# Performance work log

Hardware: AMD Instinct MI355X
Metric: run time of the kernel (lower is better)

Reference implementation:

```python
import jax, jax.numpy as jnp
import numpy as np

B, L, I, O = 32, 512, 1024, 1024
TMIN, TMAX = -8.0, -2.0


def setup_inputs() -> dict:
    key = jax.random.key(0)
    k1, k2, k3, k4, k5 = jax.random.split(key, 5)
    x = jax.random.normal(k1, (B, L, I), dtype=jnp.float32)
    weight_mean = jax.random.normal(k2, (O, I), dtype=jnp.float32) * 0.02
    # matches torch init: -rand * (tmax - tmin) + tmin
    weight_logvar = -jax.random.uniform(k3, (O, I), dtype=jnp.float32) * (TMAX - TMIN) + TMIN
    bias = jax.random.normal(k4, (O,), dtype=jnp.float32) * 0.02
    # standard-normal reparameterization noise (the torch module's randn)
    noise = jax.random.normal(k5, (B, O, I), dtype=jnp.float32)
    return {"x": x, "weight_mean": weight_mean, "weight_logvar": weight_logvar,
            "bias": bias, "noise": noise}


def reference(x, weight_mean, weight_logvar, bias, noise):
    # per-sample sampled weights: W_b = mean + eps_b * sqrt(exp(logvar))
    w = weight_mean + noise * jnp.exp(0.5 * weight_logvar)  # (B, O, I)
    # bmm(x, W^T) + bias  ->  (B, L, O)
    return jnp.einsum('bli,boi->blo', x, w) + bias
```

## Files before the change

kernel.cpp:

```cpp
#include <hip/hip_runtime.h>
#include <hip/hip_bf16.h>
#include <stdint.h>

#define B_ 32
#define L_ 512
#define I_ 1024
#define O_ 1024
#define NST 32

typedef float  f32x4 __attribute__((ext_vector_type(4)));
typedef float  f32x2 __attribute__((ext_vector_type(2)));
typedef __bf16 bf16x4 __attribute__((ext_vector_type(4)));
typedef __bf16 bf16x8 __attribute__((ext_vector_type(8)));

#define CFENCE() asm volatile("" ::: "memory")
#define BARRIER() do { CFENCE(); __builtin_amdgcn_s_barrier(); CFENCE(); } while (0)
#define LGKM0()  asm volatile("s_waitcnt lgkmcnt(0)" ::: "memory")

__global__ void gen_ms_kernel(const float* __restrict__ wmean, const float* __restrict__ wlv,
                              __bf16* __restrict__ mz, __bf16* __restrict__ sgm)
{
    const int i = blockIdx.x * blockDim.x + threadIdx.x;
    const f32x4 m = *(const f32x4*)(wmean + (size_t)i * 4);
    const f32x4 l = *(const f32x4*)(wlv   + (size_t)i * 4);
    bf16x4 mb, sb;
    #pragma unroll
    for (int e = 0; e < 4; ++e) {
        mb[e] = (__bf16)m[e];
        sb[e] = (__bf16)__expf(0.5f * l[e]);
    }
    *(bf16x4*)(mz  + (size_t)i * 4) = mb;
    *(bf16x4*)(sgm + (size_t)i * 4) = sb;
}

__global__ __launch_bounds__(256, 2) void fused_gemm(const float* __restrict__ x,
                                                     const float* __restrict__ noise,
                                                     const __bf16* __restrict__ mz,
                                                     const __bf16* __restrict__ sgm,
                                                     const float* __restrict__ bias,
                                                     float* __restrict__ out)
{
    __shared__ __align__(16) char smem[33280];

    const int bid = ((int)blockIdx.x & 7) * 128 + ((int)blockIdx.x >> 3);
    const int b   = bid >> 5;
    const int mt  = (bid >> 3) & 3;
    const int nt  = bid & 7;

    const int tid  = threadIdx.x;
    const int wave = tid >> 6, lane = tid & 63;
    const int wr   = wave >> 1;
    const int wc   = wave & 1;
    const int hr   = lane & 15;
    const int kq   = lane >> 4;

    const int r1 = tid >> 2, kc = tid & 3;
    const float*  xg = x     + ((size_t)b * L_ + mt * 128 + r1) * I_ + kc * 8;
    const float*  ng = noise + ((size_t)b * O_ + nt * 128 + r1) * I_ + kc * 8;
    const __bf16* mg = mz    + (size_t)(nt * 128 + r1) * I_ + kc * 8;
    const __bf16* gg = sgm   + (size_t)(nt * 128 + r1) * I_ + kc * 8;
    const size_t H64 = (size_t)64 * I_;
    const int wb = tid * 16;

    f32x4 sa0, sa1, sa2, sa3;
    f32x4 sn0, sn1, sn2, sn3;
    bf16x8 sm0, sm1, sg0, sg1;

#define ISSUE(k0_) do {                                      \
        sa0 = *(const f32x4*)(xg + (k0_));                   \
        sa1 = *(const f32x4*)(xg + (k0_) + 4);               \
        sa2 = *(const f32x4*)(xg + (k0_) + H64);             \
        sa3 = *(const f32x4*)(xg + (k0_) + H64 + 4);         \
        sn0 = *(const f32x4*)(ng + (k0_));                   \
        sn1 = *(const f32x4*)(ng + (k0_) + 4);               \
        sn2 = *(const f32x4*)(ng + (k0_) + H64);             \
        sn3 = *(const f32x4*)(ng + (k0_) + H64 + 4);         \
        sm0 = *(const bf16x8*)(mg + (k0_));                  \
        sm1 = *(const bf16x8*)(mg + (k0_) + H64);            \
        sg0 = *(const bf16x8*)(gg + (k0_));                  \
        sg1 = *(const bf16x8*)(gg + (k0_) + H64);            \
    } while (0)

#define TW(d_) do {                                                         \
        bf16x8 a0_, a1_, w0_, w1_;                                          \
        _Pragma("unroll")                                                   \
        for (int e = 0; e < 4; ++e) {                                       \
            a0_[e]   = (__bf16)sa0[e];  a0_[e+4] = (__bf16)sa1[e];          \
            a1_[e]   = (__bf16)sa2[e];  a1_[e+4] = (__bf16)sa3[e];          \
            w0_[e]   = (__bf16)((float)sm0[e]   + sn0[e] * (float)sg0[e]);  \
            w0_[e+4] = (__bf16)((float)sm0[e+4] + sn1[e] * (float)sg0[e+4]);\
            w1_[e]   = (__bf16)((float)sm1[e]   + sn2[e] * (float)sg1[e]);  \
            w1_[e+4] = (__bf16)((float)sm1[e+4] + sn3[e] * (float)sg1[e+4]);\
        }                                                                   \
        *(bf16x8*)(smem + (d_) * 16384 + wb)               = a0_;           \
        *(bf16x8*)(smem + (d_) * 16384 + wb + 4096)        = a1_;           \
        *(bf16x8*)(smem + (d_) * 16384 + 8192 + wb)        = w0_;           \
        *(bf16x8*)(smem + (d_) * 16384 + 8192 + wb + 4096) = w1_;           \
    } while (0)

    int aoff[4], boff[4];
    #pragma unroll
    for (int f = 0; f < 4; ++f) {
        aoff[f] = (wr * 64 + f * 16 + hr) * 64 + kq * 16;
        boff[f] = 8192 + (wc * 64 + f * 16 + hr) * 64 + kq * 16;
    }

    f32x4 acc[4][4];
    #pragma unroll
    for (int m = 0; m < 4; ++m)
        #pragma unroll
        for (int n = 0; n < 4; ++n)
            acc[m][n] = (f32x4)(0.0f);

    ISSUE(0);
    TW(0);
    ISSUE(32);
    LGKM0();
    BARRIER();

    for (int t = 0; t < NST; ++t) {
        const char* base = smem + (t & 1) * 16384;

        bf16x8 af[4], bfr[4];
        #pragma unroll
        for (int f = 0; f < 4; ++f) {
            af[f]  = *(const bf16x8*)(base + aoff[f]);
            bfr[f] = *(const bf16x8*)(base + boff[f]);
        }

        __builtin_amdgcn_s_setprio(1);
        #pragma unroll
        for (int m = 0; m < 4; ++m)
            #pragma unroll
            for (int n = 0; n < 4; ++n)
                acc[m][n] = __builtin_amdgcn_mfma_f32_16x16x32_bf16(af[m], bfr[n], acc[m][n], 0, 0, 0);
        __builtin_amdgcn_s_setprio(0);

        if (t + 1 < NST) TW((t + 1) & 1);
        if (t + 2 < NST) ISSUE((t + 2) * 32);
        LGKM0();
        BARRIER();
    }
#undef ISSUE
#undef TW

    {
        float* eb = (float*)smem;
        const f32x2 bias2 = *(const f32x2*)(bias + nt * 128 + lane * 2);
        float* ob = out + ((size_t)b * L_ + mt * 128) * O_ + nt * 128;
        #pragma unroll
        for (int r = 0; r < 2; ++r) {
            BARRIER();
            if (wr == r) {
                #pragma unroll
                for (int m = 0; m < 4; ++m)
                    #pragma unroll
                    for (int n = 0; n < 4; ++n) {
                        const int col = wc * 64 + n * 16 + hr;
                        #pragma unroll
                        for (int j = 0; j < 4; ++j)
                            eb[(m * 16 + kq * 4 + j) * 130 + col] = acc[m][n][j];
                    }
            }
            LGKM0();
            BARRIER();
            #pragma unroll
            for (int rr = 0; rr < 16; ++rr) {
                const int row = wave * 16 + rr;
                f32x2 v = *(const f32x2*)&eb[row * 130 + lane * 2];
                v[0] += bias2[0]; v[1] += bias2[1];
                *(f32x2*)&ob[(size_t)(r * 64 + row) * O_ + lane * 2] = v;
            }
        }
    }
}

#define LDSPAD 40
__global__ void bayes_gemm_fused(const float* __restrict__ x,
                                 const float* __restrict__ wmean,
                                 const float* __restrict__ wlogvar,
                                 const float* __restrict__ bias,
                                 const float* __restrict__ noise,
                                 float* __restrict__ out)
{
    __shared__ __bf16 As[128 * LDSPAD];
    __shared__ __bf16 Bs[128 * LDSPAD];
    const int bid  = blockIdx.x;
    const int b    = bid >> 5;
    const int mt   = (bid >> 3) & 3;
    const int nt   = bid & 7;
    const int t    = threadIdx.x;
    const int wave = t >> 6, lane = t & 63;
    const int wr   = wave >> 1, wc = wave & 1;
    const int hr   = lane & 15, kq = lane >> 4;
    const float* xb = x     + (size_t)b * L_ * I_;
    const float* nb = noise + (size_t)b * O_ * I_;
    f32x4 acc[4][4];
    #pragma unroll
    for (int m = 0; m < 4; ++m)
        #pragma unroll
        for (int n = 0; n < 4; ++n) acc[m][n] = (f32x4)(0.0f);
    for (int k0 = 0; k0 < I_; k0 += 32) {
        #pragma unroll
        for (int j = 0; j < 4; ++j) {
            const int s = t + j * 256, row = s >> 3, q = s & 7;
            const float4 v = *(const float4*)(xb + (size_t)(mt * 128 + row) * I_ + k0 + q * 4);
            __bf16* dst = &As[row * LDSPAD + q * 4];
            dst[0] = (__bf16)v.x; dst[1] = (__bf16)v.y; dst[2] = (__bf16)v.z; dst[3] = (__bf16)v.w;
        }
        #pragma unroll
        for (int j = 0; j < 4; ++j) {
            const int s = t + j * 256, row = s >> 3, q = s & 7;
            const size_t off = (size_t)(nt * 128 + row) * I_ + k0 + q * 4;
            const float4 m4 = *(const float4*)(wmean + off);
            const float4 l4 = *(const float4*)(wlogvar + off);
            const float4 n4 = *(const float4*)(nb + off);
            __bf16* dst = &Bs[row * LDSPAD + q * 4];
            dst[0] = (__bf16)(m4.x + n4.x * __expf(0.5f * l4.x));
            dst[1] = (__bf16)(m4.y + n4.y * __expf(0.5f * l4.y));
            dst[2] = (__bf16)(m4.z + n4.z * __expf(0.5f * l4.z));
            dst[3] = (__bf16)(m4.w + n4.w * __expf(0.5f * l4.w));
        }
        __syncthreads();
        bf16x8 af[4], bfr[4];
        #pragma unroll
        for (int m = 0; m < 4; ++m)
            af[m] = *(const bf16x8*)&As[(wr * 64 + m * 16 + hr) * LDSPAD + kq * 8];
        #pragma unroll
        for (int n = 0; n < 4; ++n)
            bfr[n] = *(const bf16x8*)&Bs[(wc * 64 + n * 16 + hr) * LDSPAD + kq * 8];
        #pragma unroll
        for (int m = 0; m < 4; ++m)
            #pragma unroll
            for (int n = 0; n < 4; ++n)
                acc[m][n] = __builtin_amdgcn_mfma_f32_16x16x32_bf16(af[m], bfr[n], acc[m][n], 0, 0, 0);
        __syncthreads();
    }
    float* ob = out + (size_t)b * L_ * O_;
    #pragma unroll
    for (int n = 0; n < 4; ++n) {
        const int col = nt * 128 + wc * 64 + n * 16 + hr;
        const float bv = bias[col];
        #pragma unroll
        for (int m = 0; m < 4; ++m) {
            const int row0 = mt * 128 + wr * 64 + m * 16 + kq * 4;
            #pragma unroll
            for (int j = 0; j < 4; ++j)
                ob[(size_t)(row0 + j) * O_ + col] = acc[m][n][j] + bv;
        }
    }
}

extern "C" void kernel_launch(void* const* d_in, const int* in_sizes, int n_in,
                              void* d_out, int out_size, void* d_ws, size_t ws_size,
                              hipStream_t stream) {
    const float* x       = (const float*)d_in[0];
    const float* wmean   = (const float*)d_in[1];
    const float* wlogvar = (const float*)d_in[2];
    const float* bias    = (const float*)d_in[3];
    const float* noise   = (const float*)d_in[4];
    float* out           = (float*)d_out;

    const size_t ms_bytes = (size_t)O_ * I_ * 2 * 2;

    if (ws_size >= ms_bytes) {
        __bf16* mzb = (__bf16*)d_ws;
        __bf16* sgb = mzb + (size_t)O_ * I_;
        gen_ms_kernel<<<dim3(O_ * I_ / 4 / 256), dim3(256), 0, stream>>>(wmean, wlogvar, mzb, sgb);
        fused_gemm<<<dim3(1024), dim3(256), 0, stream>>>(x, noise, mzb, sgb, bias, out);
    } else {
        bayes_gemm_fused<<<dim3(1024), dim3(256), 0, stream>>>(
            x, wmean, wlogvar, bias, noise, out);
    }
}
```

Before: 116.7 us.

## Split GEMM into producer and consumer waves with triple-buffered LDS and wider N tile

Replaces the 256-thread double-buffered GEMM with a 768-thread warp-specialized kernel. Four producer waves load x and noise, form the sampled bf16 weights and write them into a three-slot LDS ring. Eight consumer waves run only MFMAs on a 128x256 tile. The intent is to overlap global loads and weight synthesis with matrix math, and to halve the number of blocks, which cuts redundant x reads. In exchange, occupancy drops to one block per CU with 72KB of LDS, and the producer waves must keep up with the MFMA rate.

Result: slower. 258.2 us (+121.3%).

```diff
diff --git a/kernel.cpp b/kernel.cpp
--- a/kernel.cpp
+++ b/kernel.cpp
@@ -6,10 +6,9 @@
 #define L_ 512
 #define I_ 1024
 #define O_ 1024
-#define NST 32
+#define NWIN 32
 
 typedef float  f32x4 __attribute__((ext_vector_type(4)));
-typedef float  f32x2 __attribute__((ext_vector_type(2)));
 typedef __bf16 bf16x4 __attribute__((ext_vector_type(4)));
 typedef __bf16 bf16x8 __attribute__((ext_vector_type(8)));
 
@@ -33,78 +32,33 @@
     *(bf16x4*)(sgm + (size_t)i * 4) = sb;
 }
 
-__global__ __launch_bounds__(256, 2) void fused_gemm(const float* __restrict__ x,
-                                                     const float* __restrict__ noise,
-                                                     const __bf16* __restrict__ mz,
-                                                     const __bf16* __restrict__ sgm,
-                                                     const float* __restrict__ bias,
-                                                     float* __restrict__ out)
+__global__ __launch_bounds__(768, 1) void fused_pc(const float* __restrict__ x,
+                                                   const float* __restrict__ noise,
+                                                   const __bf16* __restrict__ mz,
+                                                   const __bf16* __restrict__ sgm,
+                                                   const float* __restrict__ bias,
+                                                   float* __restrict__ out)
 {
-    __shared__ __align__(16) char smem[33280];
-
-    const int bid = ((int)blockIdx.x & 7) * 128 + ((int)blockIdx.x >> 3);
-    const int b   = bid >> 5;
-    const int mt  = (bid >> 3) & 3;
-    const int nt  = bid & 7;
+    __shared__ __align__(16) char smem[73728];
+
+    const int bid = ((int)blockIdx.x & 7) * 64 + ((int)blockIdx.x >> 3);
+    const int b   = bid >> 4;
+    const int mt  = (bid >> 2) & 3;
+    const int nt  = bid & 3;
 
     const int tid  = threadIdx.x;
-    const int wave = tid >> 6, lane = tid & 63;
-    const int wr   = wave >> 1;
-    const int wc   = wave & 1;
+    const int wid  = tid >> 6, lane = tid & 63;
     const int hr   = lane & 15;
     const int kq   = lane >> 4;
 
-    const int r1 = tid >> 2, kc = tid & 3;
-    const float*  xg = x     + ((size_t)b * L_ + mt * 128 + r1) * I_ + kc * 8;
-    const float*  ng = noise + ((size_t)b * O_ + nt * 128 + r1) * I_ + kc * 8;
-    const __bf16* mg = mz    + (size_t)(nt * 128 + r1) * I_ + kc * 8;
-    const __bf16* gg = sgm   + (size_t)(nt * 128 + r1) * I_ + kc * 8;
-    const size_t H64 = (size_t)64 * I_;
-    const int wb = tid * 16;
-
-    f32x4 sa0, sa1, sa2, sa3;
-    f32x4 sn0, sn1, sn2, sn3;
-    bf16x8 sm0, sm1, sg0, sg1;
-
-#define ISSUE(k0_) do {                                      \
-        sa0 = *(const f32x4*)(xg + (k0_));                   \
-        sa1 = *(const f32x4*)(xg + (k0_) + 4);               \
-        sa2 = *(const f32x4*)(xg + (k0_) + H64);             \
-        sa3 = *(const f32x4*)(xg + (k0_) + H64 + 4);         \
-        sn0 = *(const f32x4*)(ng + (k0_));                   \
-        sn1 = *(const f32x4*)(ng + (k0_) + 4);               \
-        sn2 = *(const f32x4*)(ng + (k0_) + H64);             \
-        sn3 = *(const f32x4*)(ng + (k0_) + H64 + 4);         \
-        sm0 = *(const bf16x8*)(mg + (k0_));                  \
-        sm1 = *(const bf16x8*)(mg + (k0_) + H64);            \
-        sg0 = *(const bf16x8*)(gg + (k0_));                  \
-        sg1 = *(const bf16x8*)(gg + (k0_) + H64);            \
-    } while (0)
-
-#define TW(d_) do {                                                         \
-        bf16x8 a0_, a1_, w0_, w1_;                                          \
-        _Pragma("unroll")                                                   \
-        for (int e = 0; e < 4; ++e) {                                       \
-            a0_[e]   = (__bf16)sa0[e];  a0_[e+4] = (__bf16)sa1[e];          \
-            a1_[e]   = (__bf16)sa2[e];  a1_[e+4] = (__bf16)sa3[e];          \
-            w0_[e]   = (__bf16)((float)sm0[e]   + sn0[e] * (float)sg0[e]);  \
-            w0_[e+4] = (__bf16)((float)sm0[e+4] + sn1[e] * (float)sg0[e+4]);\
-            w1_[e]   = (__bf16)((float)sm1[e]   + sn2[e] * (float)sg1[e]);  \
-            w1_[e+4] = (__bf16)((float)sm1[e+4] + sn3[e] * (float)sg1[e+4]);\
-        }                                                                   \
-        *(bf16x8*)(smem + (d_) * 16384 + wb)               = a0_;           \
-        *(bf16x8*)(smem + (d_) * 16384 + wb + 4096)        = a1_;           \
-        *(bf16x8*)(smem + (d_) * 16384 + 8192 + wb)        = w0_;           \
-        *(bf16x8*)(smem + (d_) * 16384 + 8192 + wb + 4096) = w1_;           \
-    } while (0)
-
+    const int wr = (wid >> 2) & 1;
+    const int wc = wid & 3;
     int aoff[4], boff[4];
     #pragma unroll
     for (int f = 0; f < 4; ++f) {
         aoff[f] = (wr * 64 + f * 16 + hr) * 64 + kq * 16;
         boff[f] = 8192 + (wc * 64 + f * 16 + hr) * 64 + kq * 16;
     }
-
     f32x4 acc[4][4];
     #pragma unroll
     for (int m = 0; m < 4; ++m)
@@ -112,46 +66,111 @@
         for (int n = 0; n < 4; ++n)
             acc[m][n] = (f32x4)(0.0f);
 
-    ISSUE(0);
-    TW(0);
-    ISSUE(32);
-    LGKM0();
+    const int pl = (tid - 512) & 255;
+    const int rA = pl >> 2, kc = pl & 3;
+    const size_t R64 = (size_t)64 * I_;
+    const float*  xg = x     + ((size_t)b * L_ + mt * 128 + rA) * I_ + kc * 8;
+    const float*  ng = noise + ((size_t)b * O_ + nt * 256 + rA) * I_ + kc * 8;
+    const __bf16* mg = mz    + (size_t)(nt * 256 + rA) * I_ + kc * 8;
+    const __bf16* gg = sgm   + (size_t)(nt * 256 + rA) * I_ + kc * 8;
+    const int wbA = rA * 64 + kc * 16;
+    const int wbB = 8192 + rA * 64 + kc * 16;
+
+    f32x4 sa0, sa1, sa2, sa3;
+    f32x4 sn0, sn1, sn2, sn3, sn4, sn5, sn6, sn7;
+    bf16x8 sm0, sm1, sm2, sm3, sg0, sg1, sg2, sg3;
+
+#define PISSUE(ko_) do {                                                 \
+        sa0 = *(const f32x4*)(xg + (ko_));                               \
+        sa1 = *(const f32x4*)(xg + (ko_) + 4);                           \
+        sa2 = *(const f32x4*)(xg + (ko_) + R64);                         \
+        sa3 = *(const f32x4*)(xg + (ko_) + R64 + 4);                     \
+        sn0 = *(const f32x4*)(ng + (ko_));                               \
+        sn1 = *(const f32x4*)(ng + (ko_) + 4);                           \
+        sn2 = *(const f32x4*)(ng + (ko_) + R64);                         \
+        sn3 = *(const f32x4*)(ng + (ko_) + R64 + 4);                     \
+        sn4 = *(const f32x4*)(ng + (ko_) + 2 * R64);                     \
+        sn5 = *(const f32x4*)(ng + (ko_) + 2 * R64 + 4);                 \
+        sn6 = *(const f32x4*)(ng + (ko_) + 3 * R64);                     \
+        sn7 = *(const f32x4*)(ng + (ko_) + 3 * R64 + 4);                 \
+        sm0 = *(const bf16x8*)(mg + (ko_));                              \
+        sm1 = *(const bf16x8*)(mg + (ko_) + R64);                        \
+        sm2 = *(const bf16x8*)(mg + (ko_) + 2 * R64);                    \
+        sm3 = *(const bf16x8*)(mg + (ko_) + 3 * R64);                    \
+        sg0 = *(const bf16x8*)(gg + (ko_));                              \
+        sg1 = *(const bf16x8*)(gg + (ko_) + R64);                        \
+        sg2 = *(const bf16x8*)(gg + (ko_) + 2 * R64);                    \
+        sg3 = *(const bf16x8*)(gg + (ko_) + 3 * R64);                    \
+    } while (0)
+
+#define CVW(dst, smv, nlo, nhi, sgv) do {                                \
+        bf16x8 t_;                                                       \
+        _Pragma("unroll")                                                \
+        for (int e = 0; e < 4; ++e) {                                    \
+            t_[e]   = (__bf16)((float)(smv)[e]   + (nlo)[e] * (float)(sgv)[e]);   \
+            t_[e+4] = (__bf16)((float)(smv)[e+4] + (nhi)[e] * (float)(sgv)[e+4]); \
+        }                                                                \
+        *(bf16x8*)(dst) = t_;                                            \
+    } while (0)
+
+#define PWRITE(slot_) do {                                               \
+        bf16x8 a0_, a1_;                                                 \
+        _Pragma("unroll")                                                \
+        for (int e = 0; e < 4; ++e) {                                    \
+            a0_[e] = (__bf16)sa0[e]; a0_[e+4] = (__bf16)sa1[e];          \
+            a1_[e] = (__bf16)sa2[e]; a1_[e+4] = (__bf16)sa3[e];          \
+        }                                                                \
+        *(bf16x8*)(smem + (slot_) + wbA)        = a0_;                   \
+        *(bf16x8*)(smem + (slot_) + wbA + 4096) = a1_;                   \
+        CVW(smem + (slot_) + wbB,           sm0, sn0, sn1, sg0);         \
+        CVW(smem + (slot_) + wbB + 4096,    sm1, sn2, sn3, sg1);         \
+        CVW(smem + (slot_) + wbB + 8192,    sm2, sn4, sn5, sg2);         \
+        CVW(smem + (slot_) + wbB + 12288,   sm3, sn6, sn7, sg3);         \
+    } while (0)
+
+    if (wid >= 8) {
+        PISSUE(0);   PWRITE(0);
+        PISSUE(32);  PWRITE(24576);
+        PISSUE(64);
+        LGKM0();
+    }
     BARRIER();
 
-    for (int t = 0; t < NST; ++t) {
-        const char* base = smem + (t & 1) * 16384;
-
-        bf16x8 af[4], bfr[4];
-        #pragma unroll
-        for (int f = 0; f < 4; ++f) {
-            af[f]  = *(const bf16x8*)(base + aoff[f]);
-            bfr[f] = *(const bf16x8*)(base + boff[f]);
-        }
-
-        __builtin_amdgcn_s_setprio(1);
-        #pragma unroll
-        for (int m = 0; m < 4; ++m)
-            #pragma unroll
-            for (int n = 0; n < 4; ++n)
-                acc[m][n] = __builtin_amdgcn_mfma_f32_16x16x32_bf16(af[m], bfr[n], acc[m][n], 0, 0, 0);
-        __builtin_amdgcn_s_setprio(0);
-
-        if (t + 1 < NST) TW((t + 1) & 1);
-        if (t + 2 < NST) ISSUE((t + 2) * 32);
-        LGKM0();
+    for (int w = 0; w < NWIN; ++w) {
+        if (wid < 8) {
+            const char* base = smem + (w % 3) * 24576;
+            bf16x8 af[4], bfr[4];
+            #pragma unroll
+            for (int f = 0; f < 4; ++f) {
+                af[f]  = *(const bf16x8*)(base + aoff[f]);
+                bfr[f] = *(const bf16x8*)(base + boff[f]);
+            }
+            __builtin_amdgcn_s_setprio(1);
+            #pragma unroll
+            for (int m = 0; m < 4; ++m)
+                #pragma unroll
+                for (int n = 0; n < 4; ++n)
+                    acc[m][n] = __builtin_amdgcn_mfma_f32_16x16x32_bf16(af[m], bfr[n], acc[m][n], 0, 0, 0);
+            __builtin_amdgcn_s_setprio(0);
+        } else {
+            if (w + 2 < NWIN) PWRITE(((w + 2) % 3) * 24576);
+            if (w + 3 < NWIN) PISSUE((w + 3) * 32);
+            LGKM0();
+        }
         BARRIER();
     }
-#undef ISSUE
-#undef TW
+#undef PISSUE
+#undef CVW
+#undef PWRITE
 
     {
         float* eb = (float*)smem;
-        const f32x2 bias2 = *(const f32x2*)(bias + nt * 128 + lane * 2);
-        float* ob = out + ((size_t)b * L_ + mt * 128) * O_ + nt * 128;
+        const f32x4 bias4 = *(const f32x4*)(bias + nt * 256 + lane * 4);
+        float* ob = out + ((size_t)b * L_ + mt * 128) * O_ + nt * 256;
         #pragma unroll
         for (int r = 0; r < 2; ++r) {
             BARRIER();
-            if (wr == r) {
+            if (wid < 8 && wr == r) {
                 #pragma unroll
                 for (int m = 0; m < 4; ++m)
                     #pragma unroll
@@ -159,17 +178,19 @@
                         const int col = wc * 64 + n * 16 + hr;
                         #pragma unroll
                         for (int j = 0; j < 4; ++j)
-                            eb[(m * 16 + kq * 4 + j) * 130 + col] = acc[m][n][j];
+                            eb[(m * 16 + kq * 4 + j) * 260 + col] = acc[m][n][j];
                     }
             }
             LGKM0();
             BARRIER();
-            #pragma unroll
-            for (int rr = 0; rr < 16; ++rr) {
-                const int row = wave * 16 + rr;
-                f32x2 v = *(const f32x2*)&eb[row * 130 + lane * 2];
-                v[0] += bias2[0]; v[1] += bias2[1];
-                *(f32x2*)&ob[(size_t)(r * 64 + row) * O_ + lane * 2] = v;
+            if (wid < 8) {
+                #pragma unroll
+                for (int rr = 0; rr < 8; ++rr) {
+                    const int row = wid * 8 + rr;
+                    f32x4 v = *(const f32x4*)&eb[row * 260 + lane * 4];
+                    v += bias4;
+                    *(f32x4*)&ob[(size_t)(r * 64 + row) * O_ + lane * 4] = v;
+                }
             }
         }
     }
@@ -267,7 +288,7 @@
         __bf16* mzb = (__bf16*)d_ws;
         __bf16* sgb = mzb + (size_t)O_ * I_;
         gen_ms_kernel<<<dim3(O_ * I_ / 4 / 256), dim3(256), 0, stream>>>(wmean, wlogvar, mzb, sgb);
-        fused_gemm<<<dim3(1024), dim3(256), 0, stream>>>(x, noise, mzb, sgb, bias, out);
+        fused_pc<<<dim3(512), dim3(768), 0, stream>>>(x, noise, mzb, sgb, bias, out);
     } else {
         bayes_gemm_fused<<<dim3(1024), dim3(256), 0, stream>>>(
             x, wmean, wlogvar, bias, noise, out);
```

## Widen GEMM tile to 128x256 with 8 waves and async LDS loads of x

Applied to the files above, without the earlier changes.

Replaces the 128x128 tile, 4-wave GEMM with a 128x256 tile using 8 waves and 512 threads. Each block now covers twice the output columns, so the A operand (x) is fetched half as often. x is copied as fp32 straight into XOR-swizzled LDS with global_load_lds, and the conversion to bf16 moves to the LDS read path. The sampled-weight B path stays register-staged, gets a swizzle, and the epilogue writes wider float4 rows. In exchange, LDS grows to 64KB per block, each step converts more A fragments, and occupancy may drop.

Result: slower. 129.1 us (+10.6%).

```diff
diff --git a/kernel.cpp b/kernel.cpp
--- a/kernel.cpp
+++ b/kernel.cpp
@@ -9,13 +9,19 @@
 #define NST 32
 
 typedef float  f32x4 __attribute__((ext_vector_type(4)));
-typedef float  f32x2 __attribute__((ext_vector_type(2)));
 typedef __bf16 bf16x4 __attribute__((ext_vector_type(4)));
 typedef __bf16 bf16x8 __attribute__((ext_vector_type(8)));
 
 #define CFENCE() asm volatile("" ::: "memory")
 #define BARRIER() do { CFENCE(); __builtin_amdgcn_s_barrier(); CFENCE(); } while (0)
 #define LGKM0()  asm volatile("s_waitcnt lgkmcnt(0)" ::: "memory")
+
+__device__ __forceinline__ void gload_lds16(const void* g, void* l) {
+    __builtin_amdgcn_global_load_lds(
+        (const __attribute__((address_space(1))) uint32_t*)(uintptr_t)g,
+        (__attribute__((address_space(3))) uint32_t*)(uint32_t)(uintptr_t)l,
+        16, 0, 0);
+}
 
 __global__ void gen_ms_kernel(const float* __restrict__ wmean, const float* __restrict__ wlv,
                               __bf16* __restrict__ mz, __bf16* __restrict__ sgm)
@@ -33,77 +39,84 @@
     *(bf16x4*)(sgm + (size_t)i * 4) = sb;
 }
 
-__global__ __launch_bounds__(256, 2) void fused_gemm(const float* __restrict__ x,
-                                                     const float* __restrict__ noise,
-                                                     const __bf16* __restrict__ mz,
-                                                     const __bf16* __restrict__ sgm,
-                                                     const float* __restrict__ bias,
-                                                     float* __restrict__ out)
+__global__ __launch_bounds__(512, 2) void fused_a(const float* __restrict__ x,
+                                                  const float* __restrict__ noise,
+                                                  const __bf16* __restrict__ mz,
+                                                  const __bf16* __restrict__ sgm,
+                                                  const float* __restrict__ bias,
+                                                  float* __restrict__ out)
 {
-    __shared__ __align__(16) char smem[33280];
-
-    const int bid = ((int)blockIdx.x & 7) * 128 + ((int)blockIdx.x >> 3);
-    const int b   = bid >> 5;
-    const int mt  = (bid >> 3) & 3;
-    const int nt  = bid & 7;
+    __shared__ __align__(16) char smem[65536];
+
+    const int bid = ((int)blockIdx.x & 7) * 64 + ((int)blockIdx.x >> 3);
+    const int b   = bid >> 4;
+    const int mt  = (bid >> 2) & 3;
+    const int nt  = bid & 3;
 
     const int tid  = threadIdx.x;
-    const int wave = tid >> 6, lane = tid & 63;
-    const int wr   = wave >> 1;
-    const int wc   = wave & 1;
+    const int wid  = tid >> 6, lane = tid & 63;
+    const int wr   = wid >> 2;
+    const int wc   = wid & 3;
     const int hr   = lane & 15;
     const int kq   = lane >> 4;
 
-    const int r1 = tid >> 2, kc = tid & 3;
-    const float*  xg = x     + ((size_t)b * L_ + mt * 128 + r1) * I_ + kc * 8;
-    const float*  ng = noise + ((size_t)b * O_ + nt * 128 + r1) * I_ + kc * 8;
-    const __bf16* mg = mz    + (size_t)(nt * 128 + r1) * I_ + kc * 8;
-    const __bf16* gg = sgm   + (size_t)(nt * 128 + r1) * I_ + kc * 8;
-    const size_t H64 = (size_t)64 * I_;
-    const int wb = tid * 16;
-
-    f32x4 sa0, sa1, sa2, sa3;
-    f32x4 sn0, sn1, sn2, sn3;
-    bf16x8 sm0, sm1, sg0, sg1;
-
-#define ISSUE(k0_) do {                                      \
-        sa0 = *(const f32x4*)(xg + (k0_));                   \
-        sa1 = *(const f32x4*)(xg + (k0_) + 4);               \
-        sa2 = *(const f32x4*)(xg + (k0_) + H64);             \
-        sa3 = *(const f32x4*)(xg + (k0_) + H64 + 4);         \
-        sn0 = *(const f32x4*)(ng + (k0_));                   \
-        sn1 = *(const f32x4*)(ng + (k0_) + 4);               \
-        sn2 = *(const f32x4*)(ng + (k0_) + H64);             \
-        sn3 = *(const f32x4*)(ng + (k0_) + H64 + 4);         \
-        sm0 = *(const bf16x8*)(mg + (k0_));                  \
-        sm1 = *(const bf16x8*)(mg + (k0_) + H64);            \
-        sg0 = *(const bf16x8*)(gg + (k0_));                  \
-        sg1 = *(const bf16x8*)(gg + (k0_) + H64);            \
+    const int rA = tid >> 3, pcA = tid & 7;
+    const int cA = pcA ^ (rA & 7);
+    const float* xg1 = x + ((size_t)b * L_ + mt * 128 + rA) * I_ + cA * 4;
+    const float* xg2 = xg1 + (size_t)64 * I_;
+
+#define STG_A(k0_, d_) do {                                            \
+        char* ab_ = smem + (d_) * 32768;                               \
+        gload_lds16(xg1 + (k0_), ab_ + tid * 16);                      \
+        gload_lds16(xg2 + (k0_), ab_ + 8192 + tid * 16);               \
     } while (0)
 
-#define TW(d_) do {                                                         \
-        bf16x8 a0_, a1_, w0_, w1_;                                          \
-        _Pragma("unroll")                                                   \
-        for (int e = 0; e < 4; ++e) {                                       \
-            a0_[e]   = (__bf16)sa0[e];  a0_[e+4] = (__bf16)sa1[e];          \
-            a1_[e]   = (__bf16)sa2[e];  a1_[e+4] = (__bf16)sa3[e];          \
-            w0_[e]   = (__bf16)((float)sm0[e]   + sn0[e] * (float)sg0[e]);  \
-            w0_[e+4] = (__bf16)((float)sm0[e+4] + sn1[e] * (float)sg0[e+4]);\
-            w1_[e]   = (__bf16)((float)sm1[e]   + sn2[e] * (float)sg1[e]);  \
-            w1_[e+4] = (__bf16)((float)sm1[e+4] + sn3[e] * (float)sg1[e+4]);\
-        }                                                                   \
-        *(bf16x8*)(smem + (d_) * 16384 + wb)               = a0_;           \
-        *(bf16x8*)(smem + (d_) * 16384 + wb + 4096)        = a1_;           \
-        *(bf16x8*)(smem + (d_) * 16384 + 8192 + wb)        = w0_;           \
-        *(bf16x8*)(smem + (d_) * 16384 + 8192 + wb + 4096) = w1_;           \
+    const int rB = tid >> 2, pcB = tid & 3;
+    const int cB = pcB ^ ((rB >> 1) & 3);
+    const float*  ng1 = noise + ((size_t)b * O_ + nt * 256 + rB) * I_ + cB * 8;
+    const float*  ng2 = ng1 + (size_t)128 * I_;
+    const __bf16* mg1 = mz  + (size_t)(nt * 256 + rB) * I_ + cB * 8;
+    const __bf16* mg2 = mg1 + (size_t)128 * I_;
+    const __bf16* gg1 = sgm + (size_t)(nt * 256 + rB) * I_ + cB * 8;
+    const __bf16* gg2 = gg1 + (size_t)128 * I_;
+    const int wbB = 16384 + rB * 64 + pcB * 16;
+
+    f32x4 sn0, sn1, sn2, sn3; bf16x8 sm0, sm1, sg0, sg1;
+
+#define B_ISSUE(k0_) do {                                              \
+        sn0 = *(const f32x4*)(ng1 + (k0_));                            \
+        sn1 = *(const f32x4*)(ng1 + (k0_) + 4);                        \
+        sn2 = *(const f32x4*)(ng2 + (k0_));                            \
+        sn3 = *(const f32x4*)(ng2 + (k0_) + 4);                        \
+        sm0 = *(const bf16x8*)(mg1 + (k0_));                           \
+        sm1 = *(const bf16x8*)(mg2 + (k0_));                           \
+        sg0 = *(const bf16x8*)(gg1 + (k0_));                           \
+        sg1 = *(const bf16x8*)(gg2 + (k0_));                           \
     } while (0)
 
-    int aoff[4], boff[4];
-    #pragma unroll
-    for (int f = 0; f < 4; ++f) {
-        aoff[f] = (wr * 64 + f * 16 + hr) * 64 + kq * 16;
-        boff[f] = 8192 + (wc * 64 + f * 16 + hr) * 64 + kq * 16;
-    }
+#define B_WRITE(d_) do {                                                     \
+        bf16x8 w0_, w1_;                                                     \
+        _Pragma("unroll")                                                    \
+        for (int e = 0; e < 4; ++e) {                                        \
+            w0_[e]   = (__bf16)((float)sm0[e]   + sn0[e] * (float)sg0[e]);   \
+            w0_[e+4] = (__bf16)((float)sm0[e+4] + sn1[e] * (float)sg0[e+4]); \
+            w1_[e]   = (__bf16)((float)sm1[e]   + sn2[e] * (float)sg1[e]);   \
+            w1_[e+4] = (__bf16)((float)sm1[e+4] + sn3[e] * (float)sg1[e+4]); \
+        }                                                                    \
+        *(bf16x8*)(smem + (d_) * 32768 + wbB)        = w0_;                  \
+        *(bf16x8*)(smem + (d_) * 32768 + wbB + 8192) = w1_;                  \
+    } while (0)
+
+    int aoff[4][2];
+    #pragma unroll
+    for (int f = 0; f < 4; ++f)
+        #pragma unroll
+        for (int j = 0; j < 2; ++j)
+            aoff[f][j] = (wr * 64 + f * 16 + hr) * 128 + (((kq * 2 + j) ^ (hr & 7)) * 16);
+    int boff[4];
+    #pragma unroll
+    for (int n = 0; n < 4; ++n)
+        boff[n] = 16384 + (wc * 64 + n * 16 + hr) * 64 + ((kq ^ ((hr >> 1) & 3)) * 16);
 
     f32x4 acc[4][4];
     #pragma unroll
@@ -112,21 +125,31 @@
         for (int n = 0; n < 4; ++n)
             acc[m][n] = (f32x4)(0.0f);
 
-    ISSUE(0);
-    TW(0);
-    ISSUE(32);
+    STG_A(0, 0);
+    B_ISSUE(0);
+    B_WRITE(0);
+    B_ISSUE(32);
     LGKM0();
-    BARRIER();
+    __syncthreads();
 
     for (int t = 0; t < NST; ++t) {
-        const char* base = smem + (t & 1) * 16384;
+        const char* base = smem + (t & 1) * 32768;
+
+        if (t + 1 < NST) STG_A((t + 1) * 32, (t + 1) & 1);
 
         bf16x8 af[4], bfr[4];
         #pragma unroll
         for (int f = 0; f < 4; ++f) {
-            af[f]  = *(const bf16x8*)(base + aoff[f]);
-            bfr[f] = *(const bf16x8*)(base + boff[f]);
-        }
+            const f32x4 lo = *(const f32x4*)(base + aoff[f][0]);
+            const f32x4 hi = *(const f32x4*)(base + aoff[f][1]);
+            bf16x8 a_;
+            #pragma unroll
+            for (int e = 0; e < 4; ++e) { a_[e] = (__bf16)lo[e]; a_[e+4] = (__bf16)hi[e]; }
+            af[f] = a_;
+        }
+        #pragma unroll
+        for (int n = 0; n < 4; ++n)
+            bfr[n] = *(const bf16x8*)(base + boff[n]);
 
         __builtin_amdgcn_s_setprio(1);
         #pragma unroll
@@ -136,40 +159,43 @@
                 acc[m][n] = __builtin_amdgcn_mfma_f32_16x16x32_bf16(af[m], bfr[n], acc[m][n], 0, 0, 0);
         __builtin_amdgcn_s_setprio(0);
 
-        if (t + 1 < NST) TW((t + 1) & 1);
-        if (t + 2 < NST) ISSUE((t + 2) * 32);
+        if (t + 1 < NST) B_WRITE((t + 1) & 1);
+        if (t + 2 < NST) B_ISSUE((t + 2) * 32);
         LGKM0();
-        BARRIER();
-    }
-#undef ISSUE
-#undef TW
+        __syncthreads();
+    }
+#undef STG_A
+#undef B_ISSUE
+#undef B_WRITE
 
     {
         float* eb = (float*)smem;
-        const f32x2 bias2 = *(const f32x2*)(bias + nt * 128 + lane * 2);
-        float* ob = out + ((size_t)b * L_ + mt * 128) * O_ + nt * 128;
-        #pragma unroll
-        for (int r = 0; r < 2; ++r) {
+        const f32x4 bias4 = *(const f32x4*)(bias + nt * 256 + lane * 4);
+        float* ob = out + ((size_t)b * L_ + mt * 128) * O_ + nt * 256;
+        #pragma unroll
+        for (int r = 0; r < 4; ++r) {
             BARRIER();
-            if (wr == r) {
+            if (wr == (r >> 1)) {
                 #pragma unroll
-                for (int m = 0; m < 4; ++m)
+                for (int m2 = 0; m2 < 2; ++m2) {
+                    const int mf = (r & 1) * 2 + m2;
                     #pragma unroll
                     for (int n = 0; n < 4; ++n) {
                         const int col = wc * 64 + n * 16 + hr;
                         #pragma unroll
                         for (int j = 0; j < 4; ++j)
-                            eb[(m * 16 + kq * 4 + j) * 130 + col] = acc[m][n][j];
+                            eb[(m2 * 16 + kq * 4 + j) * 260 + col] = acc[mf][n][j];
                     }
+                }
             }
             LGKM0();
             BARRIER();
             #pragma unroll
-            for (int rr = 0; rr < 16; ++rr) {
-                const int row = wave * 16 + rr;
-                f32x2 v = *(const f32x2*)&eb[row * 130 + lane * 2];
-                v[0] += bias2[0]; v[1] += bias2[1];
-                *(f32x2*)&ob[(size_t)(r * 64 + row) * O_ + lane * 2] = v;
+            for (int rr = 0; rr < 4; ++rr) {
+                const int row = wid * 4 + rr;
+                f32x4 v = *(const f32x4*)&eb[row * 260 + lane * 4];
+                v += bias4;
+                *(f32x4*)&ob[(size_t)(r * 32 + row) * O_ + lane * 4] = v;
             }
         }
     }
@@ -267,7 +293,7 @@
         __bf16* mzb = (__bf16*)d_ws;
         __bf16* sgb = mzb + (size_t)O_ * I_;
         gen_ms_kernel<<<dim3(O_ * I_ / 4 / 256), dim3(256), 0, stream>>>(wmean, wlogvar, mzb, sgb);
-        fused_gemm<<<dim3(1024), dim3(256), 0, stream>>>(x, noise, mzb, sgb, bias, out);
+        fused_a<<<dim3(512), dim3(512), 0, stream>>>(x, noise, mzb, sgb, bias, out);
     } else {
         bayes_gemm_fused<<<dim3(1024), dim3(256), 0, stream>>>(
             x, wmean, wlogvar, bias, noise, out);
```
